# Kernel tuning notes

Measured on AMD Instinct MI355X. Metric: run time of the kernel, lower is better.

Reference implementation:

```python
import jax, jax.numpy as jnp
import numpy as np
from functools import partial

P = 7          # cfg.POOLING_SIZE
SAMP = 2       # fixed sampling ratio (torchvision sampling_ratio=0 is adaptive; fixed 2 used for jit)
IM_H, IM_W = 800.0, 1216.0


def conv2d(x, w, b, pad):
    y = jax.lax.conv_general_dilated(
        x, w, window_strides=(1, 1), padding=[(pad, pad), (pad, pad)],
        dimension_numbers=("NCHW", "OIHW", "NCHW"))
    return y + b[None, :, None, None]


def upsample_add(x, y):
    # F.upsample(x, size=(H,W), mode='bilinear') + y  (align_corners=False / half-pixel)
    return jax.image.resize(x, y.shape, method="bilinear") + y


def roi_align_level(feat, rois, scale):
    """torchvision roi_align (aligned=False) of all rois on one feature map.
    feat: [B,C,H,W]; rois: [N,5] = (batch_idx, x1,y1,x2,y2) in image coords.
    Returns [N,C,P,P]."""
    B, C, H, W = feat.shape
    Hf, Wf = float(H), float(W)

    def one(roi):
        b = roi[0].astype(jnp.int32)
        img = jnp.take(feat, b, axis=0)                       # [C,H,W]
        x1, y1, x2, y2 = roi[1] * scale, roi[2] * scale, roi[3] * scale, roi[4] * scale
        rw = jnp.maximum(x2 - x1, 1.0)
        rh = jnp.maximum(y2 - y1, 1.0)
        bh, bw = rh / P, rw / P
        # sample coords per bin: [P, SAMP] -> flat [P*SAMP]
        ys = (y1 + jnp.arange(P, dtype=feat.dtype)[:, None] * bh
              + (jnp.arange(SAMP, dtype=feat.dtype)[None, :] + 0.5) * bh / SAMP).reshape(-1)
        xs = (x1 + jnp.arange(P, dtype=feat.dtype)[:, None] * bw
              + (jnp.arange(SAMP, dtype=feat.dtype)[None, :] + 0.5) * bw / SAMP).reshape(-1)
        vy = (ys >= -1.0) & (ys <= Hf)
        vx = (xs >= -1.0) & (xs <= Wf)
        yc = jnp.clip(ys, 0.0, Hf - 1.0)
        xc = jnp.clip(xs, 0.0, Wf - 1.0)
        y0 = jnp.floor(yc).astype(jnp.int32)
        x0 = jnp.floor(xc).astype(jnp.int32)
        y1i = jnp.minimum(y0 + 1, H - 1)
        x1i = jnp.minimum(x0 + 1, W - 1)
        ly = yc - y0.astype(feat.dtype)
        lx = xc - x0.astype(feat.dtype)
        hy, hx = 1.0 - ly, 1.0 - lx
        v00 = img[:, y0[:, None], x0[None, :]]                # [C, PS, PS]
        v01 = img[:, y0[:, None], x1i[None, :]]
        v10 = img[:, y1i[:, None], x0[None, :]]
        v11 = img[:, y1i[:, None], x1i[None, :]]
        val = (hy[:, None] * hx[None, :]) * v00 + (hy[:, None] * lx[None, :]) * v01 \
            + (ly[:, None] * hx[None, :]) * v10 + (ly[:, None] * lx[None, :]) * v11
        val = val * (vy[:, None] & vx[None, :]).astype(feat.dtype)
        return val.reshape(C, P, SAMP, P, SAMP).mean(axis=(2, 4))   # [C,P,P]

    return jax.vmap(one)(rois)


def setup_inputs() -> dict:
    key = jax.random.key(0)
    ks = jax.random.split(key, 24)
    B = 2
    c2 = jax.random.normal(ks[0], (B, 256, 200, 304), jnp.float32)
    c3 = jax.random.normal(ks[1], (B, 512, 100, 152), jnp.float32)
    c4 = jax.random.normal(ks[2], (B, 1024, 50, 76), jnp.float32)
    c5 = jax.random.normal(ks[3], (B, 2048, 25, 38), jnp.float32)
    # FPN params (all project to 256 channels)
    def w(k, o, i, s):
        return jax.random.normal(k, (o, i, s, s), jnp.float32) * 0.01
    w_top, b_top = w(ks[4], 256, 2048, 1), jnp.zeros((256,), jnp.float32)
    w_lat1, b_lat1 = w(ks[5], 256, 1024, 1), jnp.zeros((256,), jnp.float32)
    w_lat2, b_lat2 = w(ks[6], 256, 512, 1), jnp.zeros((256,), jnp.float32)
    w_lat3, b_lat3 = w(ks[7], 256, 256, 1), jnp.zeros((256,), jnp.float32)
    w_sm1, b_sm1 = w(ks[8], 256, 256, 3), jnp.zeros((256,), jnp.float32)
    w_sm2, b_sm2 = w(ks[9], 256, 256, 3), jnp.zeros((256,), jnp.float32)
    w_sm3, b_sm3 = w(ks[10], 256, 256, 3), jnp.zeros((256,), jnp.float32)
    # ROIs: batch idx + boxes with log-uniform sizes spanning pyramid levels 2..5
    N = 1024
    bidx = jax.random.randint(ks[11], (N,), 0, B).astype(jnp.float32)
    size = jnp.exp(jax.random.uniform(ks[12], (N,), jnp.float32,
                                      np.log(32.0), np.log(640.0)))
    ar = jnp.exp(jax.random.uniform(ks[13], (N,), jnp.float32,
                                    np.log(0.5), np.log(2.0)))
    bw_ = jnp.minimum(size * jnp.sqrt(ar), IM_W - 1)
    bh_ = jnp.minimum(size / jnp.sqrt(ar), IM_H - 1)
    x1 = jax.random.uniform(ks[14], (N,), jnp.float32) * (IM_W - bw_)
    y1 = jax.random.uniform(ks[15], (N,), jnp.float32) * (IM_H - bh_)
    rois = jnp.stack([bidx, x1, y1, x1 + bw_, y1 + bh_], axis=1)
    im_info = jnp.array([[IM_H, IM_W, 1.0]], jnp.float32)
    return dict(c2=c2, c3=c3, c4=c4, c5=c5, rois=rois, im_info=im_info,
                w_top=w_top, b_top=b_top, w_lat1=w_lat1, b_lat1=b_lat1,
                w_lat2=w_lat2, b_lat2=b_lat2, w_lat3=w_lat3, b_lat3=b_lat3,
                w_sm1=w_sm1, b_sm1=b_sm1, w_sm2=w_sm2, b_sm2=b_sm2,
                w_sm3=w_sm3, b_sm3=b_sm3)


def reference(c2, c3, c4, c5, rois, im_info,
              w_top, b_top, w_lat1, b_lat1, w_lat2, b_lat2, w_lat3, b_lat3,
              w_sm1, b_sm1, w_sm2, b_sm2, w_sm3, b_sm3):
    # --- FPN top-down pathway ---
    p5 = conv2d(c5, w_top, b_top, 0)
    p4 = conv2d(upsample_add(p5, conv2d(c4, w_lat1, b_lat1, 0)), w_sm1, b_sm1, 1)
    p3 = conv2d(upsample_add(p4, conv2d(c3, w_lat2, b_lat2, 0)), w_sm2, b_sm2, 1)
    p2 = conv2d(upsample_add(p3, conv2d(c2, w_lat3, b_lat3, 0)), w_sm3, b_sm3, 1)
    mrcnn_feats = [p2, p3, p4, p5]
    # --- _PyramidRoI_Feat (POOLING_MODE == 'align') ---
    h = rois[:, 4] - rois[:, 2] + 1.0
    w_ = rois[:, 3] - rois[:, 1] + 1.0
    lvl = jnp.round(jnp.log(jnp.sqrt(h * w_) / 224.0) + 4.0)
    lvl = jnp.clip(lvl, 2.0, 5.0)
    im_h = im_info[0, 0]
    N, C = rois.shape[0], p2.shape[1]
    out = jnp.zeros((N, C, P, P), p2.dtype)
    for i, l in enumerate(range(2, 6)):
        scale = mrcnn_feats[i].shape[2] / im_h
        feat_l = roi_align_level(mrcnn_feats[i], rois, scale)
        out = jnp.where((lvl == l)[:, None, None, None], feat_l, out)
    return out
```

## Files before the change

### kernel.cpp

```cpp
#include <hip/hip_runtime.h>
#include <math.h>

typedef __attribute__((ext_vector_type(8))) short short8;
typedef __attribute__((ext_vector_type(4))) float f32x4;
typedef __attribute__((ext_vector_type(8))) unsigned short ushort8v;

__device__ __forceinline__ ushort f2bf(float f) {
    unsigned u = __builtin_bit_cast(unsigned, f);
    u = (u + 0x7fffu + ((u >> 16) & 1u)) >> 16;
    return (ushort)u;
}
__device__ __forceinline__ float bf2f(ushort h) {
    unsigned u = ((unsigned)h) << 16;
    return __builtin_bit_cast(float, u);
}

__device__ __forceinline__ void cp16(const ushort* g, ushort* l) {
    __builtin_amdgcn_global_load_lds(
        (const __attribute__((address_space(1))) unsigned int*)g,
        (__attribute__((address_space(3))) unsigned int*)l, 16, 0, 0);
}

__device__ __forceinline__ void pair_decode(int bid, int nt, int& tile, int& mm) {
    int f16 = (nt * 2) & ~15;
    if (bid < f16) { tile = ((bid >> 4) << 3) | (bid & 7); mm = (bid >> 3) & 1; }
    else { int r = bid - f16; tile = (f16 >> 1) + (r >> 1); mm = r & 1; }
}

__global__ __launch_bounds__(256) void pack_zero_k(
    const float* __restrict__ w_top,  const float* __restrict__ w_lat1,
    const float* __restrict__ w_lat2, const float* __restrict__ w_lat3,
    const float* __restrict__ w_sm1,  const float* __restrict__ w_sm2,
    const float* __restrict__ w_sm3,
    ushort* __restrict__ wtp, ushort* __restrict__ wl1,
    ushort* __restrict__ wl2, ushort* __restrict__ wl3,
    ushort* __restrict__ ws1, ushort* __restrict__ ws2, ushort* __restrict__ ws3,
    ushort* __restrict__ T4, ushort* __restrict__ T3, ushort* __restrict__ T2)
{
    const int j = blockIdx.y;
    const int i = blockIdx.x * 256 + threadIdx.x;
    if (j < 4) {
        const float* src; ushort* dst; int n;
        if      (j == 0) { src = w_top;  dst = wtp; n = 524288; }
        else if (j == 1) { src = w_lat1; dst = wl1; n = 262144; }
        else if (j == 2) { src = w_lat2; dst = wl2; n = 131072; }
        else             { src = w_lat3; dst = wl3; n = 65536;  }
        if (i < n) dst[i] = f2bf(src[i]);
    } else if (j < 7) {
        const float* src; ushort* dst;
        if      (j == 4) { src = w_sm1; dst = ws1; }
        else if (j == 5) { src = w_sm2; dst = ws2; }
        else             { src = w_sm3; dst = ws3; }
        if (i < 589824) {
            int co  = i / 2304;
            int rem = i - co * 2304;
            int tap = rem >> 8;
            int ci  = rem & 255;
            dst[i] = f2bf(src[(size_t)co * 2304 + (size_t)ci * 9 + tap]);
        }
    } else {
        ushort* Tb; int Hp, Wp, NB, total;
        if      (j == 7) { Tb = T4; Hp = 52;  Wp = 78;  NB = 256;  total = 16384; }
        else if (j == 8) { Tb = T3; Hp = 102; Wp = 154; NB = 508;  total = 32512; }
        else             { Tb = T2; Hp = 202; Wp = 306; NB = 1012; total = 64768; }
        if (i < total) {
            const int cg = (i & 31) * 8;
            const int pb = i >> 5;
            const int n  = pb / NB;
            const int b  = pb - n * NB;
            int y, x;
            if (b < 2 * Wp) { y = (b < Wp) ? 0 : (Hp - 1); x = (b < Wp) ? b : (b - Wp); }
            else { int rem = b - 2 * Wp; y = 1 + (rem >> 1); x = (rem & 1) ? (Wp - 1) : 0; }
            ushort8v z = {0, 0, 0, 0, 0, 0, 0, 0};
            *(ushort8v*)&Tb[((size_t)n * Hp * Wp + (size_t)y * Wp + x) * 256 + cg] = z;
        }
    }
}

__global__ __launch_bounds__(256) void nchw2nhwc_all(
    const float* __restrict__ c2, const float* __restrict__ c3,
    const float* __restrict__ c4, const float* __restrict__ c5,
    ushort* __restrict__ c2t, ushort* __restrict__ c3t,
    ushort* __restrict__ c4t, ushort* __restrict__ c5t)
{
    __shared__ float tile[256][33];
    const int idx = blockIdx.x;
    const float* in; ushort* out; int C, HW, tx, cy;
    if (idx < 1900)      { in = c2; out = c2t; C = 256;  HW = 60800; tx = idx; cy = 0; }
    else if (idx < 2850) { int l = idx - 1900; in = c3; out = c3t; C = 512;  HW = 15200; tx = l % 475; cy = l / 475; }
    else if (idx < 3326) { int l = idx - 2850; in = c4; out = c4t; C = 1024; HW = 3800;  tx = l % 119; cy = l / 119; }
    else                 { int l = idx - 3326; in = c5; out = c5t; C = 2048; HW = 950;   tx = l % 30;  cy = l / 30;  }
    const int n  = blockIdx.z;
    const int c0 = cy << 8;
    const int p0 = tx << 5;
    const float* inp = in + (size_t)n * C * HW + (size_t)c0 * HW + p0;
    const int t = threadIdx.x;
    const int pr = t & 31, cr = t >> 5;
    const bool pok = (p0 + pr) < HW;
    #pragma unroll 8
    for (int i = 0; i < 32; ++i) {
        int c = i * 8 + cr;
        tile[c][pr] = pok ? inp[(size_t)c * HW + pr] : 0.f;
    }
    __syncthreads();
    ushort* op = out + (size_t)n * HW * C + c0;
    const int cp = (t & 127) * 2, ph = t >> 7;
    #pragma unroll 4
    for (int j = 0; j < 16; ++j) {
        int p = j * 2 + ph;
        if (p0 + p < HW) {
            ushort2 v;
            v.x = f2bf(tile[cp][p]);
            v.y = f2bf(tile[cp + 1][p]);
            *(ushort2*)&op[(size_t)(p0 + p) * C + cp] = v;
        }
    }
}

template<int UPADD>
__global__ __launch_bounds__(256, 4) void conv1_mfma(
    const ushort* __restrict__ X, const ushort* __restrict__ Wt,
    const float* __restrict__ bias, ushort* __restrict__ Y,
    const ushort* __restrict__ Pn,
    int Cin, int H, int Wd, int nP)
{
    const int HW = H * Wd;
    int tile, mm;
    pair_decode(blockIdx.x, nP, tile, mm);
    const int p0 = tile * 128;
    const int m0 = mm << 7;
    const int n  = blockIdx.z;
    const ushort* Xn = X + (size_t)n * HW * Cin;

    const int t    = threadIdx.x;
    const int lane = t & 63;
    const int wave = t >> 6;
    const int l15  = lane & 15, lq = lane >> 4;

    __shared__ __align__(16) ushort smem[17408];

    const int rA  = ((t >> 6) << 4) | (t & 15);
    const int lq8 = ((t >> 4) & 3) * 8;
    const ushort* agA = Wt + (size_t)(m0 + rA) * Cin + lq8;
    const ushort* agB = agA + (size_t)64 * Cin;
    const ushort* XqA = Xn + (size_t)(p0 + rA) * Cin + lq8;
    const ushort* XqB = Xn + (size_t)(p0 + rA + 64) * Cin + lq8;

    const int fr    = (lq * 16 + l15) * 8;
    const int aoff  = ((wave >> 1) * 4) * 512;
    const int boff  = 4096 + ((wave & 1) * 4) * 512;
    const int wbase = wave << 9;

    const int nch = Cin >> 5;

    auto stage = [&](int bb, int c) {
        const int kA = c << 5;
        cp16(agA + kA, &smem[bb + wbase]);
        cp16(agB + kA, &smem[bb + 2048 + wbase]);
        cp16(XqA + kA, &smem[bb + 4096 + wbase]);
        cp16(XqB + kA, &smem[bb + 6144 + wbase]);
    };

    f32x4 acc[4][4] = {};

    stage(0, 0);
    __syncthreads();

    #pragma unroll 1
    for (int c = 0; c < nch; c += 2) {
        {
            stage(8192, c + 1);
            short8 af[4], bf[4];
            #pragma unroll
            for (int mi = 0; mi < 4; ++mi) af[mi] = *(const short8*)&smem[aoff + mi * 512 + fr];
            #pragma unroll
            for (int ni = 0; ni < 4; ++ni) bf[ni] = *(const short8*)&smem[boff + ni * 512 + fr];
            #pragma unroll
            for (int mi = 0; mi < 4; ++mi)
                #pragma unroll
                for (int ni = 0; ni < 4; ++ni)
                    acc[mi][ni] = __builtin_amdgcn_mfma_f32_16x16x32_bf16(
                        af[mi], bf[ni], acc[mi][ni], 0, 0, 0);
            __syncthreads();
        }
        {
            if (c + 2 < nch) stage(0, c + 2);
            short8 af[4], bf[4];
            #pragma unroll
            for (int mi = 0; mi < 4; ++mi) af[mi] = *(const short8*)&smem[8192 + aoff + mi * 512 + fr];
            #pragma unroll
            for (int ni = 0; ni < 4; ++ni) bf[ni] = *(const short8*)&smem[8192 + boff + ni * 512 + fr];
            #pragma unroll
            for (int mi = 0; mi < 4; ++mi)
                #pragma unroll
                for (int ni = 0; ni < 4; ++ni)
                    acc[mi][ni] = __builtin_amdgcn_mfma_f32_16x16x32_bf16(
                        af[mi], bf[ni], acc[mi][ni], 0, 0, 0);
            __syncthreads();
        }
    }

    const int wm = (wave >> 1) * 64, wn = (wave & 1) * 64;
    #pragma unroll
    for (int mi = 0; mi < 4; ++mi) {
        const int co = wm + mi * 16 + lq * 4;
        float4 bv = *(const float4*)&bias[m0 + co];
        float bb4[4] = {bv.x, bv.y, bv.z, bv.w};
        #pragma unroll
        for (int ni = 0; ni < 4; ++ni) {
            const int p = wn + ni * 16 + l15;
            ushort4 h;
            h.x = f2bf(acc[mi][ni][0] + bb4[0]);
            h.y = f2bf(acc[mi][ni][1] + bb4[1]);
            h.z = f2bf(acc[mi][ni][2] + bb4[2]);
            h.w = f2bf(acc[mi][ni][3] + bb4[3]);
            *(ushort4*)&smem[p * 136 + co] = h;
        }
    }
    __syncthreads();

    ushort* Yn = UPADD ? (Y + (size_t)n * (H + 2) * (Wd + 2) * 256)
                       : (Y + (size_t)n * HW * 256);
    #pragma unroll
    for (int it = 0; it < 8; ++it) {
        int idx = it * 256 + t;
        int px  = idx >> 4;
        int off = (idx & 15) * 8;
        int qq  = p0 + px;
        if (qq >= HW) continue;
        uint4 v = *(const uint4*)&smem[px * 136 + off];
        if (UPADD) {
            const int yq = qq / Wd, xq = qq - (qq / Wd) * Wd;
            const int Hh = H >> 1, Wh = Wd >> 1;
            float sy = fminf(fmaxf(yq * 0.5f - 0.25f, 0.f), (float)(Hh - 1));
            float sx = fminf(fmaxf(xq * 0.5f - 0.25f, 0.f), (float)(Wh - 1));
            int y0 = (int)sy, x0 = (int)sx;
            int y1 = min(y0 + 1, Hh - 1), x1 = min(x0 + 1, Wh - 1);
            float fy = sy - (float)y0, fx = sx - (float)x0;
            const ushort* base = Pn + (size_t)n * Hh * Wh * 256 + m0 + off;
            ushort8v a00 = *(const ushort8v*)&base[(size_t)(y0 * Wh + x0) * 256];
            ushort8v a01 = *(const ushort8v*)&base[(size_t)(y0 * Wh + x1) * 256];
            ushort8v a10 = *(const ushort8v*)&base[(size_t)(y1 * Wh + x0) * 256];
            ushort8v a11 = *(const ushort8v*)&base[(size_t)(y1 * Wh + x1) * 256];
            ushort8v tv = __builtin_bit_cast(ushort8v, v);
            ushort8v r;
            #pragma unroll
            for (int jj = 0; jj < 8; ++jj) {
                float up = (1.f - fy) * ((1.f - fx) * bf2f(a00[jj]) + fx * bf2f(a01[jj]))
                         +        fy  * ((1.f - fx) * bf2f(a10[jj]) + fx * bf2f(a11[jj]));
                r[jj] = f2bf(bf2f(tv[jj]) + up);
            }
            *(uint4*)&Yn[((size_t)(yq + 1) * (Wd + 2) + (xq + 1)) * 256 + m0 + off] =
                __builtin_bit_cast(uint4, r);
        } else {
            *(uint4*)&Yn[(size_t)qq * 256 + m0 + off] = v;
        }
    }
}

__global__ __launch_bounds__(256, 4) void conv3_mfma(
    const ushort* __restrict__ X, const ushort* __restrict__ Wt,
    const float* __restrict__ bias, ushort* __restrict__ Y,
    int Hout, int Wout, int ct, int nt)
{
    const int Wp = Wout + 2;
    int tile, mm;
    pair_decode(blockIdx.x, nt, tile, mm);
    const int ty = tile / ct, tx = tile - ty * ct;
    int y0 = ty * 8;  if (y0 > Hout - 8)  y0 = Hout - 8;
    int x0 = tx * 16; if (x0 > Wout - 16) x0 = Wout - 16;
    const int m0 = mm << 7;
    const int nb = blockIdx.z;
    const ushort* Xn = X + (size_t)nb * (Hout + 2) * Wp * 256;

    const int t    = threadIdx.x;
    const int lane = t & 63;
    const int wave = t >> 6;
    const int l15  = lane & 15, lq = lane >> 4;

    __shared__ __align__(16) ushort smem[19712];
    const int A0o = 0, A1o = 4096, B0o = 8192, B1o = 13952;

    const int rA  = ((t >> 6) << 4) | (t & 15);
    const int lq8 = ((t >> 4) & 3) * 8;
    const ushort* agA = Wt + (size_t)(m0 + rA) * 2304 + lq8;
    const ushort* agB = agA + (size_t)64 * 2304;

    const int fr   = (lq * 16 + l15) * 8;
    const int aoff = (wave >> 1) * 2048;
    const int bb   = (((wave & 1) * 16 + lq) * 144) + l15 * 8;

    auto stageA = [&](int ab, int cc, int tap) {
        const int kA = tap * 256 + (cc << 5);
        cp16(agA + kA, &smem[ab + t * 8]);
        cp16(agB + kA, &smem[ab + 2048 + t * 8]);
    };
    auto stageB = [&](int bbuf, int cc) {
        const int cb = cc << 5;
        #pragma unroll
        for (int rnd = 0; rnd < 3; ++rnd) {
            int s = rnd * 256 + t;
            if (s < 720) {
                int py  = s / 72, rem = s - py * 72;
                int lqq = rem / 18, pxc = rem - lqq * 18;
                cp16(Xn + ((size_t)(y0 + py) * Wp + (x0 + pxc)) * 256 + cb + lqq * 8,
                     &smem[bbuf + s * 8]);
            }
        }
    };

    f32x4 acc[4][4] = {};

    stageB(B0o, 0);
    stageA(A0o, 0, 0);
    __syncthreads();

    #pragma unroll 1
    for (int cc = 0; cc < 8; ++cc) {
        const int pb = cc & 1;
        const int Bb = pb ? B1o : B0o;
        #pragma unroll
        for (int tap = 0; tap < 9; ++tap) {
            const int pa = pb ^ (tap & 1);
            const int Ab = pa ? A1o : A0o;
            const int An = pa ? A0o : A1o;
            if (tap < 8) stageA(An, cc, tap + 1);
            else if (cc < 7) { stageB(pb ? B0o : B1o, cc + 1); stageA(An, cc + 1, 0); }
            const int dy = tap / 3, dx = tap - dy * 3;
            short8 af[4], bf[4];
            #pragma unroll
            for (int mi = 0; mi < 4; ++mi) af[mi] = *(const short8*)&smem[Ab + aoff + mi * 512 + fr];
            #pragma unroll
            for (int ni = 0; ni < 4; ++ni) bf[ni] = *(const short8*)&smem[Bb + bb + (ni + dy) * 576 + dx * 8];
            #pragma unroll
            for (int mi = 0; mi < 4; ++mi)
                #pragma unroll
                for (int ni = 0; ni < 4; ++ni)
                    acc[mi][ni] = __builtin_amdgcn_mfma_f32_16x16x32_bf16(
                        af[mi], bf[ni], acc[mi][ni], 0, 0, 0);
            __syncthreads();
        }
    }

    const int wm = (wave >> 1) * 64, wn = (wave & 1) * 64;
    #pragma unroll
    for (int mi = 0; mi < 4; ++mi) {
        const int co = wm + mi * 16 + lq * 4;
        float4 bv = *(const float4*)&bias[m0 + co];
        float bb4[4] = {bv.x, bv.y, bv.z, bv.w};
        #pragma unroll
        for (int ni = 0; ni < 4; ++ni) {
            const int p = wn + ni * 16 + l15;
            ushort4 h;
            h.x = f2bf(acc[mi][ni][0] + bb4[0]);
            h.y = f2bf(acc[mi][ni][1] + bb4[1]);
            h.z = f2bf(acc[mi][ni][2] + bb4[2]);
            h.w = f2bf(acc[mi][ni][3] + bb4[3]);
            *(ushort4*)&smem[p * 136 + co] = h;
        }
    }
    __syncthreads();

    ushort* Yn = Y + (size_t)nb * Hout * Wout * 256;
    #pragma unroll
    for (int it = 0; it < 8; ++it) {
        int idx = it * 256 + t;
        int p   = idx >> 4;
        int off = (idx & 15) * 8;
        int yy  = y0 + (p >> 4), xx = x0 + (p & 15);
        *(uint4*)&Yn[((size_t)yy * Wout + xx) * 256 + m0 + off] =
            *(const uint4*)&smem[p * 136 + off];
    }
}

__global__ __launch_bounds__(256) void roi_align_k(
    const float* __restrict__ rois, const float* __restrict__ im_info,
    const ushort* __restrict__ p2, const ushort* __restrict__ p3,
    const ushort* __restrict__ p4, const ushort* __restrict__ p5,
    float* __restrict__ out)
{
    const int r   = blockIdx.x;
    const int tid = threadIdx.x;

    __shared__ int   s_y0[14], s_y1[14], s_x0[14], s_x1[14];
    __shared__ float s_ly[14], s_lx[14], s_vy[14], s_vx[14];
    __shared__ float s_o[256 * 49];

    const float bx  = rois[r * 5 + 0];
    const float x1r = rois[r * 5 + 1];
    const float y1r = rois[r * 5 + 2];
    const float x2r = rois[r * 5 + 3];
    const float y2r = rois[r * 5 + 4];

    const float hh = y2r - y1r + 1.f;
    const float ww = x2r - x1r + 1.f;
    float lf = rintf(logf(sqrtf(hh * ww) * (1.f / 224.f)) + 4.f);
    lf = fminf(fmaxf(lf, 2.f), 5.f);
    const int lvl = (int)lf;

    const ushort* feat; int H, W;
    if      (lvl == 2) { feat = p2; H = 200; W = 304; }
    else if (lvl == 3) { feat = p3; H = 100; W = 152; }
    else if (lvl == 4) { feat = p4; H = 50;  W = 76;  }
    else               { feat = p5; H = 25;  W = 38;  }

    const float im_h  = im_info[0];
    const float scale = (float)H / im_h;
    const float x1 = x1r * scale, y1 = y1r * scale;
    const float x2 = x2r * scale, y2 = y2r * scale;
    const float rw = fmaxf(x2 - x1, 1.f);
    const float rh = fmaxf(y2 - y1, 1.f);
    const float bh = rh * (1.f / 7.f);
    const float bw = rw * (1.f / 7.f);

    if (tid < 28) {
        if (tid < 14) {
            int i = tid, pi = i >> 1, s = i & 1;
            float ys = y1 + pi * bh + (s + 0.5f) * bh * 0.5f;
            float v  = (ys >= -1.f && ys <= (float)H) ? 1.f : 0.f;
            float yc = fminf(fmaxf(ys, 0.f), (float)H - 1.f);
            int y0 = (int)floorf(yc);
            s_y0[i] = y0; s_y1[i] = min(y0 + 1, H - 1);
            s_ly[i] = yc - (float)y0; s_vy[i] = v;
        } else {
            int i = tid - 14, pi = i >> 1, s = i & 1;
            float xs = x1 + pi * bw + (s + 0.5f) * bw * 0.5f;
            float v  = (xs >= -1.f && xs <= (float)W) ? 1.f : 0.f;
            float xc = fminf(fmaxf(xs, 0.f), (float)W - 1.f);
            int x0 = (int)floorf(xc);
            s_x0[i] = x0; s_x1[i] = min(x0 + 1, W - 1);
            s_lx[i] = xc - (float)x0; s_vx[i] = v;
        }
    }
    __syncthreads();

    const int b = (int)bx;
    const ushort* fc = feat + (size_t)b * H * W * 256 + tid;

    #pragma unroll
    for (int py = 0; py < 7; ++py) {
        #pragma unroll
        for (int px = 0; px < 7; ++px) {
            float acc = 0.f;
            #pragma unroll
            for (int sy = 0; sy < 2; ++sy) {
                #pragma unroll
                for (int sx = 0; sx < 2; ++sx) {
                    int iy = py * 2 + sy, ix = px * 2 + sx;
                    float ly = s_ly[iy], lx = s_lx[ix];
                    float hy = 1.f - ly, hx = 1.f - lx;
                    int y0 = s_y0[iy], y1i = s_y1[iy];
                    int x0 = s_x0[ix], x1i = s_x1[ix];
                    float v00 = bf2f(fc[(size_t)(y0 * W + x0) * 256]);
                    float v01 = bf2f(fc[(size_t)(y0 * W + x1i) * 256]);
                    float v10 = bf2f(fc[(size_t)(y1i * W + x0) * 256]);
                    float v11 = bf2f(fc[(size_t)(y1i * W + x1i) * 256]);
                    float val = hy * hx * v00 + hy * lx * v01
                              + ly * hx * v10 + ly * lx * v11;
                    acc += val * s_vy[iy] * s_vx[ix];
                }
            }
            s_o[tid * 49 + py * 7 + px] = acc * 0.25f;
        }
    }
    __syncthreads();
    float* orow = out + (size_t)r * 256 * 49;
    for (int it = 0; it < 49; ++it)
        orow[it * 256 + tid] = s_o[it * 256 + tid];
}

static inline int cdiv(int a, int b) { return (a + b - 1) / b; }

extern "C" void kernel_launch(void* const* d_in, const int* in_sizes, int n_in,
                              void* d_out, int out_size, void* d_ws, size_t ws_size,
                              hipStream_t stream) {
    const float* c2      = (const float*)d_in[0];
    const float* c3      = (const float*)d_in[1];
    const float* c4      = (const float*)d_in[2];
    const float* c5      = (const float*)d_in[3];
    const float* rois    = (const float*)d_in[4];
    const float* im_info = (const float*)d_in[5];
    const float* w_top   = (const float*)d_in[6];
    const float* b_top   = (const float*)d_in[7];
    const float* w_lat1  = (const float*)d_in[8];
    const float* b_lat1  = (const float*)d_in[9];
    const float* w_lat2  = (const float*)d_in[10];
    const float* b_lat2  = (const float*)d_in[11];
    const float* w_lat3  = (const float*)d_in[12];
    const float* b_lat3  = (const float*)d_in[13];
    const float* w_sm1   = (const float*)d_in[14];
    const float* b_sm1   = (const float*)d_in[15];
    const float* w_sm2   = (const float*)d_in[16];
    const float* b_sm2   = (const float*)d_in[17];
    const float* w_sm3   = (const float*)d_in[18];
    const float* b_sm3   = (const float*)d_in[19];
    float* out = (float*)d_out;
    ushort* ws = (ushort*)d_ws;

    ushort* c2t = ws;
    ushort* c3t = c2t + 31129600;
    ushort* c4t = c3t + 15564800;
    ushort* c5t = c4t + 7782400;
    ushort* p5  = c5t + 3891200;
    ushort* p4  = p5  + 486400;
    ushort* p3  = p4  + 1945600;
    ushort* T2  = p3  + 7782400;
    ushort* T3  = T2  + 31647744;
    ushort* T4  = T3  + 8042496;
    ushort* wtp = T4  + 2076672;
    ushort* wl1 = wtp + 524288;
    ushort* wl2 = wl1 + 262144;
    ushort* wl3 = wl2 + 131072;
    ushort* ws1 = wl3 + 65536;
    ushort* ws2 = ws1 + 589824;
    ushort* ws3 = ws2 + 589824;
    ushort* p2  = c2t;

    dim3 blk(256);

    pack_zero_k<<<dim3(2304, 10), blk, 0, stream>>>(
        w_top, w_lat1, w_lat2, w_lat3, w_sm1, w_sm2, w_sm3,
        wtp, wl1, wl2, wl3, ws1, ws2, ws3, T4, T3, T2);

    nchw2nhwc_all<<<dim3(3566, 1, 2), blk, 0, stream>>>(
        c2, c3, c4, c5, c2t, c3t, c4t, c5t);

    conv1_mfma<0><<<dim3(16, 1, 2), blk, 0, stream>>>(c5t, wtp, b_top, p5, (const ushort*)0, 2048, 25, 38, 8);

    conv1_mfma<1><<<dim3(60, 1, 2), blk, 0, stream>>>(c4t, wl1, b_lat1, T4, p5, 1024, 50, 76, 30);
    conv3_mfma<<<dim3(70, 1, 2), blk, 0, stream>>>(T4, ws1, b_sm1, p4, 50, 76, 5, 35);

    conv1_mfma<1><<<dim3(238, 1, 2), blk, 0, stream>>>(c3t, wl2, b_lat2, T3, p4, 512, 100, 152, 119);
    conv3_mfma<<<dim3(260, 1, 2), blk, 0, stream>>>(T3, ws2, b_sm2, p3, 100, 152, 10, 130);

    conv1_mfma<1><<<dim3(950, 1, 2), blk, 0, stream>>>(c2t, wl3, b_lat3, T2, p3, 256, 200, 304, 475);
    conv3_mfma<<<dim3(950, 1, 2), blk, 0, stream>>>(T2, ws3, b_sm3, p2, 200, 304, 19, 475);

    roi_align_k<<<dim3(1024), blk, 0, stream>>>(rois, im_info, p2, p3, p4, p5, out);
}
```

Baseline: 1.019 ms.

## Vectorize RoIAlign gathers to 4 channels per thread and pad shared output

The RoIAlign kernel now has each thread handle 4 contiguous channels, loaded as 8-byte ushort4 values, with the 256 threads split into 4 bin groups that stride over the 49 output bins. Before, each thread loaded one 2-byte channel per sample. The shared output buffer is transposed to a bin-major layout padded to 260 floats per bin, and the final global store reads it transposed. The aim is wider, better-coalesced gather loads, bilinear weights computed once per sample rather than per channel, and fewer shared-memory bank conflicts. In exchange the final copy adds integer division and strided shared reads.

```diff
diff --git a/kernel.cpp b/kernel.cpp
--- a/kernel.cpp
+++ b/kernel.cpp
@@ -384,7 +384,7 @@
 
     __shared__ int   s_y0[14], s_y1[14], s_x0[14], s_x1[14];
     __shared__ float s_ly[14], s_lx[14], s_vy[14], s_vx[14];
-    __shared__ float s_o[256 * 49];
+    __shared__ float s_o[49 * 260];
 
     const float bx  = rois[r * 5 + 0];
     const float x1r = rois[r * 5 + 1];
@@ -434,39 +434,48 @@
     }
     __syncthreads();
 
-    const int b = (int)bx;
-    const ushort* fc = feat + (size_t)b * H * W * 256 + tid;
-
-    #pragma unroll
-    for (int py = 0; py < 7; ++py) {
+    const int b  = (int)bx;
+    const int cg = tid & 63;
+    const int bg = tid >> 6;
+    const ushort* fc = feat + (size_t)b * H * W * 256 + cg * 4;
+
+    for (int bin = bg; bin < 49; bin += 4) {
+        const int py = bin / 7, px = bin - (bin / 7) * 7;
+        f32x4 acc = {0.f, 0.f, 0.f, 0.f};
         #pragma unroll
-        for (int px = 0; px < 7; ++px) {
-            float acc = 0.f;
-            #pragma unroll
-            for (int sy = 0; sy < 2; ++sy) {
-                #pragma unroll
-                for (int sx = 0; sx < 2; ++sx) {
-                    int iy = py * 2 + sy, ix = px * 2 + sx;
-                    float ly = s_ly[iy], lx = s_lx[ix];
-                    float hy = 1.f - ly, hx = 1.f - lx;
-                    int y0 = s_y0[iy], y1i = s_y1[iy];
-                    int x0 = s_x0[ix], x1i = s_x1[ix];
-                    float v00 = bf2f(fc[(size_t)(y0 * W + x0) * 256]);
-                    float v01 = bf2f(fc[(size_t)(y0 * W + x1i) * 256]);
-                    float v10 = bf2f(fc[(size_t)(y1i * W + x0) * 256]);
-                    float v11 = bf2f(fc[(size_t)(y1i * W + x1i) * 256]);
-                    float val = hy * hx * v00 + hy * lx * v01
-                              + ly * hx * v10 + ly * lx * v11;
-                    acc += val * s_vy[iy] * s_vx[ix];
-                }
+        for (int sy = 0; sy < 2; ++sy) {
+            #pragma unroll
+            for (int sx = 0; sx < 2; ++sx) {
+                const int iy = py * 2 + sy, ix = px * 2 + sx;
+                const float ly = s_ly[iy], lx = s_lx[ix];
+                const float hy = 1.f - ly, hx = 1.f - lx;
+                const int y0 = s_y0[iy], y1i = s_y1[iy];
+                const int x0 = s_x0[ix], x1i = s_x1[ix];
+                const float vf  = s_vy[iy] * s_vx[ix];
+                const float w00 = hy * hx * vf, w01 = hy * lx * vf;
+                const float w10 = ly * hx * vf, w11 = ly * lx * vf;
+                ushort4 u00 = *(const ushort4*)&fc[(size_t)(y0 * W + x0) * 256];
+                ushort4 u01 = *(const ushort4*)&fc[(size_t)(y0 * W + x1i) * 256];
+                ushort4 u10 = *(const ushort4*)&fc[(size_t)(y1i * W + x0) * 256];
+                ushort4 u11 = *(const ushort4*)&fc[(size_t)(y1i * W + x1i) * 256];
+                acc[0] += w00 * bf2f(u00.x) + w01 * bf2f(u01.x) + w10 * bf2f(u10.x) + w11 * bf2f(u11.x);
+                acc[1] += w00 * bf2f(u00.y) + w01 * bf2f(u01.y) + w10 * bf2f(u10.y) + w11 * bf2f(u11.y);
+                acc[2] += w00 * bf2f(u00.z) + w01 * bf2f(u01.z) + w10 * bf2f(u10.z) + w11 * bf2f(u11.z);
+                acc[3] += w00 * bf2f(u00.w) + w01 * bf2f(u01.w) + w10 * bf2f(u10.w) + w11 * bf2f(u11.w);
             }
-            s_o[tid * 49 + py * 7 + px] = acc * 0.25f;
-        }
-    }
-    __syncthreads();
+        }
+        acc[0] *= 0.25f; acc[1] *= 0.25f; acc[2] *= 0.25f; acc[3] *= 0.25f;
+        *(f32x4*)&s_o[bin * 260 + cg * 4] = acc;
+    }
+    __syncthreads();
+
     float* orow = out + (size_t)r * 256 * 49;
-    for (int it = 0; it < 49; ++it)
-        orow[it * 256 + tid] = s_o[it * 256 + tid];
+    for (int it = 0; it < 49; ++it) {
+        int j  = it * 256 + tid;
+        int c  = j / 49;
+        int bq = j - c * 49;
+        orow[j] = s_o[bq * 260 + c];
+    }
 }
 
 static inline int cdiv(int a, int b) { return (a + b - 1) / b; }
```

Measured after the change: 879.5 us. 13.7% less time.
